# Optimization experiments

Measured on AMD Instinct MI355X. Metric: run time of the kernel, lower is better.

## Reference

```python
import jax, jax.numpy as jnp
import numpy as np

B, S, D = 1, 2048, 1024
NH, NKV, HD = 16, 4, 64
N_REP = NH // NKV


def _rope_tables(seq_len, half_dim, base=10000.0):
    inv_freq = 1.0 / (base ** (np.arange(0, half_dim, dtype=np.float32) / half_dim))
    t = np.arange(seq_len, dtype=np.float32)
    freqs = np.outer(t, inv_freq)  # (S, HD//2)
    return jnp.asarray(np.cos(freqs)), jnp.asarray(np.sin(freqs))


def setup_inputs() -> dict:
    key = jax.random.key(0)
    ks = jax.random.split(key, 5)
    x = jax.random.normal(ks[0], (B, S, D), dtype=jnp.float32)
    rope_cos, rope_sin = _rope_tables(S, HD // 2)
    sd = 1.0 / np.sqrt(D)
    Wq = jax.random.normal(ks[1], (D, NH * HD), dtype=jnp.float32) * sd
    Wk = jax.random.normal(ks[2], (D, NKV * HD), dtype=jnp.float32) * sd
    Wv = jax.random.normal(ks[3], (D, NKV * HD), dtype=jnp.float32) * sd
    Wo = jax.random.normal(ks[4], (NH * HD, D), dtype=jnp.float32) * sd
    return {"x": x, "rope_cos": rope_cos, "rope_sin": rope_sin,
            "Wq": Wq, "Wk": Wk, "Wv": Wv, "Wo": Wo}


def _apply_rope(t, cos, sin):
    # t: (B, H, S, HD); cos/sin: (S, HD//2). Rotate-half convention.
    t1, t2 = jnp.split(t, 2, axis=-1)
    c = cos[None, None, :, :]
    s = sin[None, None, :, :]
    return jnp.concatenate([t1 * c - t2 * s, t2 * c + t1 * s], axis=-1)


def reference(x, rope_cos, rope_sin, Wq, Wk, Wv, Wo):
    b, s, _ = x.shape
    # projections -> (B, H, S, HD)
    q = (x @ Wq).reshape(b, s, NH, HD).transpose(0, 2, 1, 3)
    k = (x @ Wk).reshape(b, s, NKV, HD).transpose(0, 2, 1, 3)
    v = (x @ Wv).reshape(b, s, NKV, HD).transpose(0, 2, 1, 3)
    q = _apply_rope(q, rope_cos, rope_sin)
    k = _apply_rope(k, rope_cos, rope_sin)
    # GQA expansion (repeat_interleave on head axis)
    k = jnp.repeat(k, N_REP, axis=1)
    v = jnp.repeat(v, N_REP, axis=1)
    scale = HD ** -0.5
    scores = jnp.einsum('bhqd,bhkd->bhqk', q, k) * scale
    causal = jnp.tril(jnp.ones((s, s), dtype=bool))
    scores = jnp.where(causal[None, None], scores, jnp.float32(-jnp.inf))
    attn = jax.nn.softmax(scores, axis=-1)
    out = jnp.einsum('bhqk,bhkd->bhqd', attn, v)  # (B, H, S, HD)
    out = out.transpose(0, 2, 1, 3).reshape(b, s, NH * HD)
    return out @ Wo
```

## Files before the change

kernel.cpp:

```cpp
#include <hip/hip_runtime.h>

typedef unsigned short ushort_t;
typedef __attribute__((ext_vector_type(8))) short short8;
typedef __attribute__((ext_vector_type(4))) float f32x4;
typedef __attribute__((ext_vector_type(4))) unsigned short ushort4v;
typedef __attribute__((ext_vector_type(8))) unsigned short ushort8v;

#define S_LEN 2048
#define D_MODEL 1024
#define NH 16
#define NKV 4
#define HD 64

__device__ __forceinline__ ushort_t f2bf(float f) {
    unsigned u = __float_as_uint(f);
    u += 0x7fffu + ((u >> 16) & 1u);
    return (ushort_t)(u >> 16);
}

__device__ __forceinline__ void cp16(void* lds, const void* g) {
    __builtin_amdgcn_global_load_lds(
        (__attribute__((address_space(1))) void*)g,
        (__attribute__((address_space(3))) void*)lds, 16, 0, 0);
}

__global__ __launch_bounds__(256) void prep_kernel(
    const float* __restrict__ x, ushort_t* __restrict__ xb,
    const float* __restrict__ Wq, const float* __restrict__ Wk,
    const float* __restrict__ Wv, const float* __restrict__ Wo,
    ushort_t* __restrict__ WqT, ushort_t* __restrict__ WkT,
    ushort_t* __restrict__ WvT, ushort_t* __restrict__ WoT)
{
    const int t = threadIdx.x;
    if (blockIdx.z == 4) {
        const int b  = blockIdx.y * 16 + blockIdx.x;
        const int i0 = (b * 256 + t) * 4;
        #pragma unroll
        for (int rep = 0; rep < 8; ++rep) {
            const int i = i0 + rep * 262144;
            float4 v = *(const float4*)(x + i);
            ushort4v o = { f2bf(v.x), f2bf(v.y), f2bf(v.z), f2bf(v.w) };
            *(ushort4v*)(xb + i) = o;
        }
        return;
    }
    __shared__ ushort_t T[64 * 72];
    const float* W; ushort_t* WT; int N;
    switch (blockIdx.z) {
        case 0:  W = Wq; WT = WqT; N = 1024; break;
        case 1:  W = Wk; WT = WkT; N = 256;  break;
        case 2:  W = Wv; WT = WvT; N = 256;  break;
        default: W = Wo; WT = WoT; N = 1024; break;
    }
    const int n0 = blockIdx.y * 64;
    if (n0 >= N) return;
    const int k0 = blockIdx.x * 64;
    const int kr = t >> 4, nc = (t & 15) * 4;
    #pragma unroll
    for (int p = 0; p < 4; ++p) {
        const int k = kr + p * 16;
        float4 v = *(const float4*)(W + (size_t)(k0 + k) * N + n0 + nc);
        T[(nc + 0) * 72 + k] = f2bf(v.x);
        T[(nc + 1) * 72 + k] = f2bf(v.y);
        T[(nc + 2) * 72 + k] = f2bf(v.z);
        T[(nc + 3) * 72 + k] = f2bf(v.w);
    }
    __syncthreads();
    const int n = t >> 2, seg = (t & 3) * 16;
    ushort8v a = *(ushort8v*)&T[n * 72 + seg];
    ushort8v b = *(ushort8v*)&T[n * 72 + seg + 8];
    *(ushort8v*)(WT + (size_t)(n0 + n) * 1024 + k0 + seg)     = a;
    *(ushort8v*)(WT + (size_t)(n0 + n) * 1024 + k0 + seg + 8) = b;
}

__global__ __launch_bounds__(256, 3) void gemm_qkv_mfma(
    const ushort_t* __restrict__ xb, const ushort_t* __restrict__ WqT,
    const ushort_t* __restrict__ WkT, const ushort_t* __restrict__ WvT,
    const float* __restrict__ rc, const float* __restrict__ rs,
    ushort_t* __restrict__ Qb, ushort_t* __restrict__ Kb,
    ushort_t* __restrict__ Vtb)
{
    __shared__ ushort_t As[2][64 * 64];
    __shared__ ushort_t Bs[2][128 * 64];

    const int t = threadIdx.x;
    const int lane = t & 63, wave = t >> 6;
    const int wr = wave >> 1, wc = wave & 1;
    const int quad = lane >> 4, l15 = lane & 15;
    const int lq = lane >> 3, lr = lane & 7;
    const int swz_st = (lr ^ lq) * 8;
    const int l7 = l15 & 7;
    const int fsw0 = (quad ^ l7) * 8;
    const int fsw1 = ((quad + 4) ^ l7) * 8;

    const int m0 = blockIdx.x * 64;
    const int cy = blockIdx.y;

    const ushort_t* WT; int nloc;
    if (cy < 8)       { WT = WqT; nloc = cy * 128; }
    else if (cy < 10) { WT = WkT; nloc = (cy - 8) * 128; }
    else              { WT = WvT; nloc = (cy - 10) * 128; }

    f32x4 acc[2][4];
    #pragma unroll
    for (int i = 0; i < 2; ++i)
        #pragma unroll
        for (int j = 0; j < 4; ++j) acc[i][j] = (f32x4)0.f;

    auto stage = [&](int buf, int k0) {
        #pragma unroll
        for (int i = 0; i < 2; ++i) {
            const int r = wave * 16 + i * 8 + lq;
            cp16(&As[buf][(wave * 16 + i * 8) * 64],
                 xb + (size_t)(m0 + r) * 1024 + k0 + swz_st);
        }
        #pragma unroll
        for (int i = 0; i < 4; ++i) {
            const int r = wave * 32 + i * 8 + lq;
            cp16(&Bs[buf][(wave * 32 + i * 8) * 64],
                 WT + (size_t)(nloc + r) * 1024 + k0 + swz_st);
        }
    };

    stage(0, 0);
    __syncthreads();

    for (int kk = 0; kk < 16; ++kk) {
        const int cur = kk & 1;
        if (kk + 1 < 16) stage(cur ^ 1, (kk + 1) * 64);

        const ushort_t* Ac = &As[cur][0];
        const ushort_t* Bc = &Bs[cur][0];
        #pragma unroll
        for (int h = 0; h < 2; ++h) {
            const int fsw = h ? fsw1 : fsw0;
            short8 av[2], bv[4];
            #pragma unroll
            for (int i = 0; i < 2; ++i)
                av[i] = *(const short8*)&Ac[(wr * 32 + i * 16 + l15) * 64 + fsw];
            #pragma unroll
            for (int j = 0; j < 4; ++j)
                bv[j] = *(const short8*)&Bc[(wc * 64 + j * 16 + l15) * 64 + fsw];
            #pragma unroll
            for (int i = 0; i < 2; ++i)
                #pragma unroll
                for (int j = 0; j < 4; ++j)
                    acc[i][j] = __builtin_amdgcn_mfma_f32_16x16x32_bf16(
                        av[i], bv[j], acc[i][j], 0, 0, 0);
        }
        __syncthreads();
    }

    if (cy < 10) {
        ushort_t* dst = (cy < 8) ? Qb : Kb;
        const int h = ((cy < 8) ? cy : (cy - 8)) * 2 + wc;
        #pragma unroll
        for (int i = 0; i < 2; ++i) {
            #pragma unroll
            for (int j = 0; j < 2; ++j) {
                const int d = j * 16 + l15;
                #pragma unroll
                for (int reg = 0; reg < 4; ++reg) {
                    const int s = m0 + wr * 32 + i * 16 + quad * 4 + reg;
                    const float c  = rc[s * 32 + d];
                    const float sn = rs[s * 32 + d];
                    const float v1 = acc[i][j][reg];
                    const float v2 = acc[i][j + 2][reg];
                    dst[((size_t)h * S_LEN + s) * HD + d]      = f2bf(v1 * c - v2 * sn);
                    dst[((size_t)h * S_LEN + s) * HD + d + 32] = f2bf(v2 * c + v1 * sn);
                }
            }
        }
    } else {
        const int vh = (cy - 10) * 2 + wc;
        #pragma unroll
        for (int i = 0; i < 2; ++i) {
            const int s0 = m0 + wr * 32 + i * 16 + quad * 4;
            #pragma unroll
            for (int j = 0; j < 4; ++j) {
                const int d = j * 16 + l15;
                ushort4v o = { f2bf(acc[i][j][0]), f2bf(acc[i][j][1]),
                               f2bf(acc[i][j][2]), f2bf(acc[i][j][3]) };
                *(ushort4v*)&Vtb[((size_t)vh * HD + d) * S_LEN + s0] = o;
            }
        }
    }
}

__global__ __launch_bounds__(256, 2) void attn_mfma(
    const ushort_t* __restrict__ Qb, const ushort_t* __restrict__ Kb,
    const ushort_t* __restrict__ Vtb, ushort_t* __restrict__ attnb)
{
    __shared__ ushort_t Ks[2][2][64 * 64];
    __shared__ ushort_t Vs[2][2][64 * 64];
    __shared__ ushort_t Ps[4][16 * 72];

    const int t = threadIdx.x;
    const int lane = t & 63, wave = t >> 6;
    const int quad = lane >> 4, l15 = lane & 15;
    const int lq = lane >> 3, lr = lane & 7;
    const int swz_st = (lr ^ lq) * 8;
    const int l7 = l15 & 7;
    const int fsw0 = (quad ^ l7) * 8;
    const int fsw1 = ((quad + 4) ^ l7) * 8;

    const int h  = blockIdx.x;
    const int y  = blockIdx.y;
    const int qt = (y < 16) ? y : 47 - y;
    const int q0 = qt * 64;
    const int kvh = h >> 2;
    const int qrow0 = q0 + wave * 16;

    const ushort_t* Qg = Qb + ((size_t)h * S_LEN + qrow0) * HD;
    const ushort_t* Kg = Kb + (size_t)kvh * S_LEN * HD;
    const ushort_t* Vg = Vtb + (size_t)kvh * HD * S_LEN;

    short8 aq0 = *(const short8*)(Qg + (size_t)l15 * HD + quad * 8);
    short8 aq1 = *(const short8*)(Qg + (size_t)l15 * HD + 32 + quad * 8);

    float ps4[4] = {0.f, 0.f, 0.f, 0.f};
    f32x4 Oacc[4];
    #pragma unroll
    for (int jb = 0; jb < 4; ++jb) Oacc[jb] = (f32x4)0.f;

    const int nround = (qt + 2) >> 1;

    auto stage = [&](int buf, int kvbase) {
        #pragma unroll
        for (int u = 0; u < 2; ++u)
            #pragma unroll
            for (int i = 0; i < 2; ++i) {
                const int r = wave * 16 + i * 8 + lq;
                cp16(&Ks[buf][u][(wave * 16 + i * 8) * 64],
                     Kg + (size_t)(kvbase + u * 64 + r) * 64 + swz_st);
                cp16(&Vs[buf][u][(wave * 16 + i * 8) * 64],
                     Vg + (size_t)r * 2048 + kvbase + u * 64 + swz_st);
            }
    };

    stage(0, 0);
    __syncthreads();

    ushort_t* Pw = &Ps[wave][0];

    for (int round = 0; round < nround; ++round) {
        const int cur = round & 1;
        if (round + 1 < nround) stage(cur ^ 1, (round + 1) * 128);

        #pragma unroll
        for (int u = 0; u < 2; ++u) {
            const int kv0 = round * 128 + u * 64;
            if (kv0 > q0 + 63) break;
            const ushort_t* Kc = &Ks[cur][u][0];
            const ushort_t* Vc = &Vs[cur][u][0];

            f32x4 sv[4];
            #pragma unroll
            for (int jb = 0; jb < 4; ++jb) {
                short8 b0 = *(const short8*)&Kc[(jb * 16 + l15) * 64 + fsw0];
                short8 b1 = *(const short8*)&Kc[(jb * 16 + l15) * 64 + fsw1];
                f32x4 z = (f32x4)0.f;
                z = __builtin_amdgcn_mfma_f32_16x16x32_bf16(aq0, b0, z, 0, 0, 0);
                z = __builtin_amdgcn_mfma_f32_16x16x32_bf16(aq1, b1, z, 0, 0, 0);
                sv[jb] = z;
            }

            const bool diag = (kv0 == q0);
            #pragma unroll
            for (int jb = 0; jb < 4; ++jb) {
                const int col = kv0 + jb * 16 + l15;
                #pragma unroll
                for (int reg = 0; reg < 4; ++reg) {
                    float e = __expf(sv[jb][reg] * 0.125f);
                    if (diag && col > qrow0 + quad * 4 + reg) e = 0.f;
                    sv[jb][reg] = e;
                    ps4[reg] += e;
                }
            }

            #pragma unroll
            for (int jb = 0; jb < 4; ++jb)
                #pragma unroll
                for (int reg = 0; reg < 4; ++reg)
                    Pw[(quad * 4 + reg) * 72 + jb * 16 + l15] = f2bf(sv[jb][reg]);
            short8 p0 = *(const short8*)&Pw[l15 * 72 + quad * 8];
            short8 p1 = *(const short8*)&Pw[l15 * 72 + 32 + quad * 8];

            #pragma unroll
            for (int jb = 0; jb < 4; ++jb) {
                short8 v0 = *(const short8*)&Vc[(jb * 16 + l15) * 64 + fsw0];
                short8 v1 = *(const short8*)&Vc[(jb * 16 + l15) * 64 + fsw1];
                Oacc[jb] = __builtin_amdgcn_mfma_f32_16x16x32_bf16(p0, v0, Oacc[jb], 0, 0, 0);
                Oacc[jb] = __builtin_amdgcn_mfma_f32_16x16x32_bf16(p1, v1, Oacc[jb], 0, 0, 0);
            }
        }

        __syncthreads();
    }

    #pragma unroll
    for (int reg = 0; reg < 4; ++reg) {
        float l = ps4[reg];
        l += __shfl_xor(l, 1);
        l += __shfl_xor(l, 2);
        l += __shfl_xor(l, 4);
        l += __shfl_xor(l, 8);
        const float inv = 1.f / l;
        const int s = qrow0 + quad * 4 + reg;
        #pragma unroll
        for (int jb = 0; jb < 4; ++jb)
            attnb[(size_t)s * D_MODEL + h * HD + jb * 16 + l15] =
                f2bf(Oacc[jb][reg] * inv);
    }
}

__global__ __launch_bounds__(256, 4) void gemm_out_mfma(
    const ushort_t* __restrict__ Ab, const ushort_t* __restrict__ WoT,
    float* __restrict__ out)
{
    __shared__ ushort_t As[2][64 * 64];
    __shared__ ushort_t Bs[2][64 * 64];

    const int t = threadIdx.x;
    const int lane = t & 63, wave = t >> 6;
    const int wr = wave >> 1, wc = wave & 1;
    const int quad = lane >> 4, l15 = lane & 15;
    const int lq = lane >> 3, lr = lane & 7;
    const int swz_st = (lr ^ lq) * 8;
    const int l7 = l15 & 7;
    const int fsw0 = (quad ^ l7) * 8;
    const int fsw1 = ((quad + 4) ^ l7) * 8;

    const int m0 = blockIdx.x * 64;
    const int n0 = blockIdx.y * 64;

    f32x4 acc[2][2];
    #pragma unroll
    for (int i = 0; i < 2; ++i)
        #pragma unroll
        for (int j = 0; j < 2; ++j) acc[i][j] = (f32x4)0.f;

    auto stage = [&](int buf, int k0) {
        #pragma unroll
        for (int i = 0; i < 2; ++i) {
            const int r = wave * 16 + i * 8 + lq;
            cp16(&As[buf][(wave * 16 + i * 8) * 64],
                 Ab + (size_t)(m0 + r) * 1024 + k0 + swz_st);
            cp16(&Bs[buf][(wave * 16 + i * 8) * 64],
                 WoT + (size_t)(n0 + r) * 1024 + k0 + swz_st);
        }
    };

    stage(0, 0);
    __syncthreads();

    for (int kk = 0; kk < 16; ++kk) {
        const int cur = kk & 1;
        if (kk + 1 < 16) stage(cur ^ 1, (kk + 1) * 64);

        const ushort_t* Ac = &As[cur][0];
        const ushort_t* Bc = &Bs[cur][0];
        #pragma unroll
        for (int h = 0; h < 2; ++h) {
            const int fsw = h ? fsw1 : fsw0;
            short8 av[2], bv[2];
            #pragma unroll
            for (int i = 0; i < 2; ++i)
                av[i] = *(const short8*)&Ac[(wr * 32 + i * 16 + l15) * 64 + fsw];
            #pragma unroll
            for (int j = 0; j < 2; ++j)
                bv[j] = *(const short8*)&Bc[(wc * 32 + j * 16 + l15) * 64 + fsw];
            #pragma unroll
            for (int i = 0; i < 2; ++i)
                #pragma unroll
                for (int j = 0; j < 2; ++j)
                    acc[i][j] = __builtin_amdgcn_mfma_f32_16x16x32_bf16(
                        av[i], bv[j], acc[i][j], 0, 0, 0);
        }
        __syncthreads();
    }

    #pragma unroll
    for (int i = 0; i < 2; ++i)
        #pragma unroll
        for (int reg = 0; reg < 4; ++reg) {
            const int s = m0 + wr * 32 + i * 16 + quad * 4 + reg;
            #pragma unroll
            for (int j = 0; j < 2; ++j)
                out[(size_t)s * D_MODEL + n0 + wc * 32 + j * 16 + l15] = acc[i][j][reg];
        }
}

extern "C" void kernel_launch(void* const* d_in, const int* in_sizes, int n_in,
                              void* d_out, int out_size, void* d_ws, size_t ws_size,
                              hipStream_t stream)
{
    const float* x  = (const float*)d_in[0];
    const float* rc = (const float*)d_in[1];
    const float* rs = (const float*)d_in[2];
    const float* Wq = (const float*)d_in[3];
    const float* Wk = (const float*)d_in[4];
    const float* Wv = (const float*)d_in[5];
    const float* Wo = (const float*)d_in[6];
    float* out = (float*)d_out;

    ushort_t* xb   = (ushort_t*)d_ws;
    ushort_t* WqT  = xb   + (size_t)2048 * 1024;
    ushort_t* WkT  = WqT  + (size_t)1024 * 1024;
    ushort_t* WvT  = WkT  + (size_t)256 * 1024;
    ushort_t* WoT  = WvT  + (size_t)256 * 1024;
    ushort_t* Qb   = WoT  + (size_t)1024 * 1024;
    ushort_t* Kb   = Qb   + (size_t)NH * S_LEN * HD;
    ushort_t* Vtb  = Kb   + (size_t)NKV * S_LEN * HD;
    ushort_t* attnb= Vtb  + (size_t)NKV * HD * S_LEN;

    prep_kernel<<<dim3(16, 16, 5), 256, 0, stream>>>(x, xb, Wq, Wk, Wv, Wo,
                                                     WqT, WkT, WvT, WoT);
    gemm_qkv_mfma<<<dim3(32, 12), 256, 0, stream>>>(xb, WqT, WkT, WvT,
                                                    rc, rs, Qb, Kb, Vtb);
    attn_mfma<<<dim3(NH, 32), 256, 0, stream>>>(Qb, Kb, Vtb, attnb);
    gemm_out_mfma<<<dim3(32, 16), 256, 0, stream>>>(attnb, WoT, out);
}
```

Measured before the change: 144.2 us.

## Compute transposed scores so P feeds PV MFMA from registers without LDS

Swaps the MFMA operands for the QK^T product so each lane holds a column of scores for one query row, letting the bf16 probabilities be packed directly into the A operand of the PV MFMA instead of going through a per-wave LDS round-trip. V fragment reads are reorganised into four 8-byte swizzled loads per block to match the new k-index ordering, and the softmax row-sum is now reduced across quads then broadcast by shuffle. This removes LDS writes/reads and the associated bank traffic for P, at the cost of more, smaller LDS reads for V.

```diff
diff --git a/kernel.cpp b/kernel.cpp
--- a/kernel.cpp
+++ b/kernel.cpp
@@ -2,6 +2,7 @@
 
 typedef unsigned short ushort_t;
 typedef __attribute__((ext_vector_type(8))) short short8;
+typedef __attribute__((ext_vector_type(4))) short short4v;
 typedef __attribute__((ext_vector_type(4))) float f32x4;
 typedef __attribute__((ext_vector_type(4))) unsigned short ushort4v;
 typedef __attribute__((ext_vector_type(8))) unsigned short ushort8v;
@@ -193,7 +194,6 @@
 {
     __shared__ ushort_t Ks[2][2][64 * 64];
     __shared__ ushort_t Vs[2][2][64 * 64];
-    __shared__ ushort_t Ps[4][16 * 72];
 
     const int t = threadIdx.x;
     const int lane = t & 63, wave = t >> 6;
@@ -204,6 +204,13 @@
     const int fsw0 = (quad ^ l7) * 8;
     const int fsw1 = ((quad + 4) ^ l7) * 8;
 
+    const int vq  = quad >> 1;
+    const int q14 = (quad & 1) << 2;
+    const int vo0 = (((0 + vq) ^ l7) << 3) + q14;
+    const int vo1 = (((2 + vq) ^ l7) << 3) + q14;
+    const int vo2 = (((4 + vq) ^ l7) << 3) + q14;
+    const int vo3 = (((6 + vq) ^ l7) << 3) + q14;
+
     const int h  = blockIdx.x;
     const int y  = blockIdx.y;
     const int qt = (y < 16) ? y : 47 - y;
@@ -218,7 +225,7 @@
     short8 aq0 = *(const short8*)(Qg + (size_t)l15 * HD + quad * 8);
     short8 aq1 = *(const short8*)(Qg + (size_t)l15 * HD + 32 + quad * 8);
 
-    float ps4[4] = {0.f, 0.f, 0.f, 0.f};
+    float psum = 0.f;
     f32x4 Oacc[4];
     #pragma unroll
     for (int jb = 0; jb < 4; ++jb) Oacc[jb] = (f32x4)0.f;
@@ -241,8 +248,6 @@
     stage(0, 0);
     __syncthreads();
 
-    ushort_t* Pw = &Ps[wave][0];
-
     for (int round = 0; round < nround; ++round) {
         const int cur = round & 1;
         if (round + 1 < nround) stage(cur ^ 1, (round + 1) * 128);
@@ -257,39 +262,45 @@
             f32x4 sv[4];
             #pragma unroll
             for (int jb = 0; jb < 4; ++jb) {
-                short8 b0 = *(const short8*)&Kc[(jb * 16 + l15) * 64 + fsw0];
-                short8 b1 = *(const short8*)&Kc[(jb * 16 + l15) * 64 + fsw1];
+                short8 k0 = *(const short8*)&Kc[(jb * 16 + l15) * 64 + fsw0];
+                short8 k1 = *(const short8*)&Kc[(jb * 16 + l15) * 64 + fsw1];
                 f32x4 z = (f32x4)0.f;
-                z = __builtin_amdgcn_mfma_f32_16x16x32_bf16(aq0, b0, z, 0, 0, 0);
-                z = __builtin_amdgcn_mfma_f32_16x16x32_bf16(aq1, b1, z, 0, 0, 0);
+                z = __builtin_amdgcn_mfma_f32_16x16x32_bf16(k0, aq0, z, 0, 0, 0);
+                z = __builtin_amdgcn_mfma_f32_16x16x32_bf16(k1, aq1, z, 0, 0, 0);
                 sv[jb] = z;
             }
 
             const bool diag = (kv0 == q0);
+            const int qg = qrow0 + l15;
             #pragma unroll
             for (int jb = 0; jb < 4; ++jb) {
-                const int col = kv0 + jb * 16 + l15;
                 #pragma unroll
                 for (int reg = 0; reg < 4; ++reg) {
                     float e = __expf(sv[jb][reg] * 0.125f);
-                    if (diag && col > qrow0 + quad * 4 + reg) e = 0.f;
+                    if (diag && (kv0 + jb * 16 + quad * 4 + reg) > qg) e = 0.f;
                     sv[jb][reg] = e;
-                    ps4[reg] += e;
+                    psum += e;
                 }
             }
 
-            #pragma unroll
-            for (int jb = 0; jb < 4; ++jb)
-                #pragma unroll
-                for (int reg = 0; reg < 4; ++reg)
-                    Pw[(quad * 4 + reg) * 72 + jb * 16 + l15] = f2bf(sv[jb][reg]);
-            short8 p0 = *(const short8*)&Pw[l15 * 72 + quad * 8];
-            short8 p1 = *(const short8*)&Pw[l15 * 72 + 32 + quad * 8];
+            short8 p0 = { (short)f2bf(sv[0][0]), (short)f2bf(sv[0][1]),
+                          (short)f2bf(sv[0][2]), (short)f2bf(sv[0][3]),
+                          (short)f2bf(sv[1][0]), (short)f2bf(sv[1][1]),
+                          (short)f2bf(sv[1][2]), (short)f2bf(sv[1][3]) };
+            short8 p1 = { (short)f2bf(sv[2][0]), (short)f2bf(sv[2][1]),
+                          (short)f2bf(sv[2][2]), (short)f2bf(sv[2][3]),
+                          (short)f2bf(sv[3][0]), (short)f2bf(sv[3][1]),
+                          (short)f2bf(sv[3][2]), (short)f2bf(sv[3][3]) };
 
             #pragma unroll
             for (int jb = 0; jb < 4; ++jb) {
-                short8 v0 = *(const short8*)&Vc[(jb * 16 + l15) * 64 + fsw0];
-                short8 v1 = *(const short8*)&Vc[(jb * 16 + l15) * 64 + fsw1];
+                const ushort_t* Vrow = &Vc[(jb * 16 + l15) * 64];
+                short4v va0 = *(const short4v*)&Vrow[vo0];
+                short4v va1 = *(const short4v*)&Vrow[vo1];
+                short4v va2 = *(const short4v*)&Vrow[vo2];
+                short4v va3 = *(const short4v*)&Vrow[vo3];
+                short8 v0 = __builtin_shufflevector(va0, va1, 0, 1, 2, 3, 4, 5, 6, 7);
+                short8 v1 = __builtin_shufflevector(va2, va3, 0, 1, 2, 3, 4, 5, 6, 7);
                 Oacc[jb] = __builtin_amdgcn_mfma_f32_16x16x32_bf16(p0, v0, Oacc[jb], 0, 0, 0);
                 Oacc[jb] = __builtin_amdgcn_mfma_f32_16x16x32_bf16(p1, v1, Oacc[jb], 0, 0, 0);
             }
@@ -298,14 +309,11 @@
         __syncthreads();
     }
 
+    psum += __shfl_xor(psum, 16);
+    psum += __shfl_xor(psum, 32);
     #pragma unroll
     for (int reg = 0; reg < 4; ++reg) {
-        float l = ps4[reg];
-        l += __shfl_xor(l, 1);
-        l += __shfl_xor(l, 2);
-        l += __shfl_xor(l, 4);
-        l += __shfl_xor(l, 8);
-        const float inv = 1.f / l;
+        const float inv = 1.f / __shfl(psum, quad * 4 + reg);
         const int s = qrow0 + quad * 4 + reg;
         #pragma unroll
         for (int jb = 0; jb < 4; ++jb)
```

Measured after the change: 145.3 us. No clear change (+0.7%).
